# Optimization experiments

Measured on AMD Instinct MI355X. Metric: run time of the kernel, lower is better.

## Reference

```python
import jax, jax.numpy as jnp
import numpy as np

NU, NM, NT = 200000, 50000, 20000   # users, movies, tags
F, H, L = 64, 128, 2                # genre feat dim, hidden, layers
E1, E2 = 800000, 400000             # rates edges, has_tag edges


def setup_inputs() -> dict:
    key = jax.random.key(0)
    ks = jax.random.split(key, 12)
    s = 1.0 / np.sqrt(H)
    return {
        "genre": jax.random.normal(ks[0], (NM, F), jnp.float32),
        "user_emb": jax.random.normal(ks[1], (NU, H), jnp.float32),
        "tag_emb": jax.random.normal(ks[2], (NT, H), jnp.float32),
        "movie_W": jax.random.normal(ks[3], (H, F), jnp.float32) * (1.0 / np.sqrt(F)),
        "movie_b": jnp.zeros((H,), jnp.float32),
        # per-layer, per-edge-type SAGEConv weights; etype order: [rates, rev_rates, has_tag, tag_of]
        "Wn": jax.random.normal(ks[4], (L, 4, H, H), jnp.float32) * s,  # fc_neigh (no bias)
        "Ws": jax.random.normal(ks[5], (L, 4, H, H), jnp.float32) * s,  # fc_self
        "bs": jnp.zeros((L, 4, H), jnp.float32),                        # fc_self bias
        "rates_u": jax.random.randint(ks[6], (E1,), 0, NU, jnp.int32),
        "rates_m": jax.random.randint(ks[7], (E1,), 0, NM, jnp.int32),
        "tag_m": jax.random.randint(ks[8], (E2,), 0, NM, jnp.int32),
        "tag_t": jax.random.randint(ks[9], (E2,), 0, NT, jnp.int32),
    }


def _sage(h_src, h_dst, src, dst, n_dst, Wn, Wself, b):
    # DGL SAGEConv('mean'): fc_self(h_dst) + fc_neigh(mean_{src->dst} h_src)
    m = h_src[src]                                                        # [E, H] gather
    ssum = jax.ops.segment_sum(m, dst, num_segments=n_dst)                # [n_dst, H]
    cnt = jax.ops.segment_sum(jnp.ones((src.shape[0], 1), h_src.dtype), dst, num_segments=n_dst)
    mean = ssum / jnp.maximum(cnt, 1.0)                                   # zero-degree -> 0
    return h_dst @ Wself.T + b + mean @ Wn.T


def reference(genre, user_emb, tag_emb, movie_W, movie_b, Wn, Ws, bs,
              rates_u, rates_m, tag_m, tag_t):
    hu = user_emb
    hm = genre @ movie_W.T + movie_b
    ht = tag_emb
    for l in range(L):
        # HeteroGraphConv(aggregate='sum'): movie receives 'rates' + 'tag_of'
        new_m = (_sage(hu, hm, rates_u, rates_m, NM, Wn[l, 0], Ws[l, 0], bs[l, 0])
                 + _sage(ht, hm, tag_t, tag_m, NM, Wn[l, 3], Ws[l, 3], bs[l, 3]))
        new_u = _sage(hm, hu, rates_m, rates_u, NU, Wn[l, 1], Ws[l, 1], bs[l, 1])  # rev_rates
        new_t = _sage(hm, ht, tag_m, tag_t, NT, Wn[l, 2], Ws[l, 2], bs[l, 2])      # has_tag
        # dropout in eval mode (identity), then LeakyReLU(0.1)
        hu = jax.nn.leaky_relu(new_u, 0.1)
        hm = jax.nn.leaky_relu(new_m, 0.1)
        ht = jax.nn.leaky_relu(new_t, 0.1)
    return hu, hm
```

## Files before the change

### kernel.cpp

```cpp
#include <hip/hip_runtime.h>
#include <stdint.h>


#define NUSR 200000
#define NMOV 50000
#define NTAG 20000
#define FDIM 64
#define HDIM 128
#define NE1  800000
#define NE2  400000

#define OFF_RM 0
#define OFF_RU (NMOV)
#define OFF_TM (NMOV + NUSR)
#define OFF_TT (NMOV + NUSR + NMOV)
#define NTOT   (2 * NMOV + NUSR + NTAG)
#define ETOT   (2 * NE1 + 2 * NE2)
#define WHH    (HDIM * HDIM)

#define WTOT (8192 + 2 * 7 * WHH)
#define BREP 768

#define NB0 196
#define NB1 196
#define NB2 98
#define NB3 157
#define NB  (NB0 + NB1 + NB2 + NB3)
#define S1_EPB 8192
#define S1_B0 98
#define S1_B1 98
#define S1_B2 49
#define S1_B3 49
#define S1_NBLK (S1_B0 + S1_B1 + S1_B2 + S1_B3)
#define CAP 6144

typedef short bf16x8 __attribute__((ext_vector_type(8)));
typedef float f32x4 __attribute__((ext_vector_type(4)));

static inline int cdiv(int a, int b) { return (a + b - 1) / b; }

__device__ __forceinline__ float bf2f(unsigned short u) {
    union { unsigned int i; float f; } c;
    c.i = ((unsigned int)u) << 16;
    return c.f;
}
__device__ __forceinline__ unsigned short f2bf(float f) {
    union { float f; unsigned int i; } c;
    c.f = f;
    unsigned int i = c.i;
    return (unsigned short)((i + 0x7fffu + ((i >> 16) & 1u)) >> 16);
}

__device__ __forceinline__ void gload_lds16(const unsigned short* g, unsigned short* l) {
    __builtin_amdgcn_global_load_lds(
        (const __attribute__((address_space(1))) unsigned int*)(g),
        (__attribute__((address_space(3))) unsigned int*)(l), 16, 0, 0);
}

struct SegInfo {
    int e0, eN, sh, sbb, nb;
    const int* dstA;
    const int* srcA;
};
__device__ __forceinline__ SegInfo seg_decode(int blk, const int* ru, const int* rm,
                                              const int* tm, const int* tt) {
    SegInfo s;
    if (blk < S1_B0) {
        s.e0 = blk * S1_EPB; s.eN = NE1; s.sh = 8;  s.sbb = 0;                 s.nb = NB0;
        s.dstA = rm; s.srcA = ru;
    } else if (blk < S1_B0 + S1_B1) {
        s.e0 = (blk - S1_B0) * S1_EPB; s.eN = NE1; s.sh = 10; s.sbb = NB0;     s.nb = NB1;
        s.dstA = ru; s.srcA = rm;
    } else if (blk < S1_B0 + S1_B1 + S1_B2) {
        s.e0 = (blk - S1_B0 - S1_B1) * S1_EPB; s.eN = NE2; s.sh = 9;
        s.sbb = NB0 + NB1; s.nb = NB2;
        s.dstA = tm; s.srcA = tt;
    } else {
        s.e0 = (blk - S1_B0 - S1_B1 - S1_B2) * S1_EPB; s.eN = NE2; s.sh = 7;
        s.sbb = NB0 + NB1 + NB2; s.nb = NB3;
        s.dstA = tt; s.srcA = tm;
    }
    return s;
}

__global__ __launch_bounds__(256) void csr_bucket_hist(const int* __restrict__ ru,
                                                       const int* __restrict__ rm,
                                                       const int* __restrict__ tm,
                                                       const int* __restrict__ tt,
                                                       int* __restrict__ bcnt) {
    __shared__ int h[256];
    const int t = threadIdx.x;
    h[t] = 0;
    __syncthreads();
    const SegInfo s = seg_decode(blockIdx.x, ru, rm, tm, tt);
#pragma unroll 4
    for (int i = 0; i < S1_EPB / 256; ++i) {
        const int e = s.e0 + t + i * 256;
        if (e < s.eN) atomicAdd(&h[s.dstA[e] >> s.sh], 1);
    }
    __syncthreads();
    if (t < s.nb) {
        const int c = h[t];
        if (c) atomicAdd(&bcnt[s.sbb + t], c);
    }
}

__global__ __launch_bounds__(1024) void csr_bscan(const int* __restrict__ bcnt,
                                                  int* __restrict__ bbase,
                                                  int* __restrict__ bcur,
                                                  int* __restrict__ rowptr) {
    __shared__ int sh[1024];
    const int t = threadIdx.x;
    const int v = (t < NB) ? bcnt[t] : 0;
    sh[t] = v;
    __syncthreads();
    for (int off = 1; off < 1024; off <<= 1) {
        const int add = (t >= off) ? sh[t - off] : 0;
        __syncthreads();
        sh[t] += add;
        __syncthreads();
    }
    const int ex = sh[t] - v;
    if (t < NB) { bbase[t] = ex; bcur[t] = ex; }
    if (t == NB - 1) bbase[NB] = ex + v;
    if (t == 0) rowptr[NTOT] = ETOT;
}

__global__ __launch_bounds__(256) void csr_bin(const int* __restrict__ ru,
                                               const int* __restrict__ rm,
                                               const int* __restrict__ tm,
                                               const int* __restrict__ tt,
                                               int* __restrict__ bcur,
                                               int* __restrict__ tmp) {
    __shared__ int h[256], st[256], gb[256], cu[256];
    __shared__ int rec[S1_EPB];
    __shared__ unsigned short bk[S1_EPB];
    const int t = threadIdx.x;
    h[t] = 0;
    __syncthreads();
    const SegInfo s = seg_decode(blockIdx.x, ru, rm, tm, tt);
    const int mask = (1 << s.sh) - 1;
#pragma unroll 4
    for (int i = 0; i < S1_EPB / 256; ++i) {
        const int e = s.e0 + t + i * 256;
        if (e < s.eN) atomicAdd(&h[s.dstA[e] >> s.sh], 1);
    }
    __syncthreads();
    const int v = h[t];
    cu[t] = v;
    __syncthreads();
    for (int off = 1; off < 256; off <<= 1) {
        const int add = (t >= off) ? cu[t - off] : 0;
        __syncthreads();
        cu[t] += add;
        __syncthreads();
    }
    st[t] = cu[t] - v;
    gb[t] = (t < s.nb && v) ? atomicAdd(&bcur[s.sbb + t], v) : 0;
    cu[t] = st[t];
    __syncthreads();
#pragma unroll 4
    for (int i = 0; i < S1_EPB / 256; ++i) {
        const int e = s.e0 + t + i * 256;
        if (e < s.eN) {
            const int d = s.dstA[e];
            const int lb = d >> s.sh;
            const int r = ((d & mask) << 18) | s.srcA[e];
            const int p = atomicAdd(&cu[lb], 1);
            rec[p] = r;
            bk[p] = (unsigned short)lb;
        }
    }
    __syncthreads();
    const int ecount = min(S1_EPB, s.eN - s.e0);
    for (int q = t; q < ecount; q += 256) {
        const int lb = bk[q];
        tmp[gb[lb] + (q - st[lb])] = rec[q];
    }
}

__global__ __launch_bounds__(256) void csr_sort(const int* __restrict__ tmp,
                                                const int* __restrict__ bbase,
                                                int* __restrict__ rowptr,
                                                int* __restrict__ sorted) {
    __shared__ int h[1024];
    __shared__ int part[256];
    __shared__ int outb[CAP];
    const int b = blockIdx.x;
    const int t = threadIdx.x;
    int c0, nctr;
    if (b < NB0)                 { c0 = OFF_RM + (b << 8);                nctr = min(256,  NMOV - (b << 8)); }
    else if (b < NB0 + NB1)      { const int j = b - NB0;                 c0 = OFF_RU + (j << 10); nctr = min(1024, NUSR - (j << 10)); }
    else if (b < NB0 + NB1 + NB2){ const int j = b - NB0 - NB1;           c0 = OFF_TM + (j << 9);  nctr = min(512,  NMOV - (j << 9)); }
    else                         { const int j = b - NB0 - NB1 - NB2;     c0 = OFF_TT + (j << 7);  nctr = min(128,  NTAG - (j << 7)); }
    for (int k = t; k < 1024; k += 256) h[k] = 0;
    __syncthreads();
    const int lo = bbase[b], hi = bbase[b + 1];
    const int n = hi - lo;
    for (int e = lo + t; e < hi; e += 256) atomicAdd(&h[tmp[e] >> 18], 1);
    __syncthreads();
    const int b4 = t * 4;
    const int a0 = h[b4], a1 = h[b4 + 1], a2 = h[b4 + 2], a3 = h[b4 + 3];
    const int sum = a0 + a1 + a2 + a3;
    part[t] = sum;
    __syncthreads();
    for (int off = 1; off < 256; off <<= 1) {
        const int add = (t >= off) ? part[t - off] : 0;
        __syncthreads();
        part[t] += add;
        __syncthreads();
    }
    int run = part[t] - sum;
    h[b4] = run; run += a0;
    h[b4 + 1] = run; run += a1;
    h[b4 + 2] = run; run += a2;
    h[b4 + 3] = run;
    __syncthreads();
    for (int k = t; k < nctr; k += 256) rowptr[c0 + k] = lo + h[k];
    __syncthreads();
    if (n <= CAP) {
        for (int e = lo + t; e < hi; e += 256) {
            const int r = tmp[e];
            const int p = atomicAdd(&h[r >> 18], 1);
            outb[p] = r & 0x3FFFF;
        }
        __syncthreads();
        for (int q = t; q < n; q += 256) sorted[lo + q] = outb[q];
    } else {
        for (int e = lo + t; e < hi; e += 256) {
            const int r = tmp[e];
            const int p = atomicAdd(&h[r >> 18], 1);
            sorted[lo + p] = r & 0x3FFFF;
        }
    }
}

__global__ __launch_bounds__(256) void prep_all(
    const float* __restrict__ i0, unsigned short* __restrict__ o0, int n0,
    const float* __restrict__ i1, unsigned short* __restrict__ o1, int n1,
    const float* __restrict__ i2, unsigned short* __restrict__ o2, int n2,
    int gcvt,
    const float* __restrict__ movie_W, const float* __restrict__ movie_b,
    const float* __restrict__ Wn, const float* __restrict__ Ws,
    const float* __restrict__ bs,
    unsigned short* __restrict__ WB, float* __restrict__ BB) {
    if ((int)blockIdx.x < gcvt) {
        int i = blockIdx.x * 256 + threadIdx.x;
        const float* in; unsigned short* out;
        if (i < n0) { in = i0; out = o0; }
        else if (i < n0 + n1) { in = i1; out = o1; i -= n0; }
        else if (i < n0 + n1 + n2) { in = i2; out = o2; i -= n0 + n1; }
        else return;
        const float4 v = ((const float4*)in)[i];
        ushort4 o;
        o.x = f2bf(v.x); o.y = f2bf(v.y); o.z = f2bf(v.z); o.w = f2bf(v.w);
        ((ushort4*)out)[i] = o;
        return;
    }
    const int i = (blockIdx.x - gcvt) * 256 + threadIdx.x;
    if (i < BREP) {
        const int seg = i >> 7, c = i & 127;
        float bv;
        if (seg == 0)      bv = movie_b[c];
        else if (seg == 1) bv = bs[0 * 512 + 1 * 128 + c];
        else if (seg == 2) bv = bs[0 * 512 + 2 * 128 + c];
        else if (seg == 3) bv = bs[0 * 512 + 0 * 128 + c] + bs[0 * 512 + 3 * 128 + c];
        else if (seg == 4) bv = bs[1 * 512 + 1 * 128 + c];
        else               bv = bs[1 * 512 + 0 * 128 + c] + bs[1 * 512 + 3 * 128 + c];
#pragma unroll
        for (int r = 0; r < 8; ++r) BB[r * BREP + i] = bv;
    }
    if (i < WTOT) {
        float v;
        int dest;
        if (i < 8192) {
            v = movie_W[i];
            const int r0 = i >> 6, c0 = i & 63;
            dest = (r0 << 6) + ((((c0 >> 3) ^ (r0 & 7)) << 3) | (c0 & 7));
        } else {
            const int j = i - 8192;
            const int l = j / (7 * WHH);
            const int rr = j % (7 * WHH);
            const int e = rr / WHH;
            const int o = rr % WHH;
            if (e < 4) v = Wn[(l * 4 + e) * WHH + o];
            else if (e == 4) v = Ws[(l * 4 + 1) * WHH + o];
            else if (e == 5) v = Ws[(l * 4 + 2) * WHH + o];
            else v = Ws[(l * 4 + 0) * WHH + o] + Ws[(l * 4 + 3) * WHH + o];
            const int r0 = o >> 7, c0 = o & 127;
            dest = 8192 + l * 7 * WHH + e * WHH +
                   (r0 << 7) + ((((c0 >> 3) ^ (r0 & 7)) << 3) | (c0 & 7));
        }
        const unsigned short bf = f2bf(v);
#pragma unroll
        for (int r = 0; r < 8; ++r) WB[(size_t)r * WTOT + dest] = bf;
    }
}

__global__ __launch_bounds__(256) void agg4(
    const unsigned short* __restrict__ f0, const int* __restrict__ rp0, unsigned short* __restrict__ o0,
    const unsigned short* __restrict__ f1, const int* __restrict__ rp1, unsigned short* __restrict__ o1,
    const unsigned short* __restrict__ f2, const int* __restrict__ rp2, unsigned short* __restrict__ o2,
    const unsigned short* __restrict__ f3, const int* __restrict__ rp3, unsigned short* __restrict__ o3,
    int c0, int c1, int c2, int c3,
    const int* __restrict__ sorted) {
    int g = blockIdx.x * 16 + (threadIdx.x >> 4);
    const unsigned short* feat; const int* rp; unsigned short* out;
    if (g < c0) { feat = f0; rp = rp0; out = o0; }
    else if (g < c1) { feat = f1; rp = rp1; out = o1; g -= c0; }
    else if (g < c2) { feat = f2; rp = rp2; out = o2; g -= c1; }
    else if (g < c3) { feat = f3; rp = rp3; out = o3; g -= c2; }
    else return;
    const int lane = threadIdx.x & 15;
    const int s = rp[g], e = rp[g + 1];
    float a[8];
#pragma unroll
    for (int k = 0; k < 8; ++k) a[k] = 0.f;
    int j = s;
    for (; j + 1 < e; j += 2) {
        const int s0 = sorted[j], s1 = sorted[j + 1];
        const bf16x8 v0 = *(const bf16x8*)&feat[(size_t)s0 * HDIM + lane * 8];
        const bf16x8 v1 = *(const bf16x8*)&feat[(size_t)s1 * HDIM + lane * 8];
#pragma unroll
        for (int k = 0; k < 8; ++k) a[k] += bf2f((unsigned short)v0[k]) + bf2f((unsigned short)v1[k]);
    }
    if (j < e) {
        const int s0 = sorted[j];
        const bf16x8 v0 = *(const bf16x8*)&feat[(size_t)s0 * HDIM + lane * 8];
#pragma unroll
        for (int k = 0; k < 8; ++k) a[k] += bf2f((unsigned short)v0[k]);
    }
    const float sc = (e > s) ? 1.0f / (float)(e - s) : 0.0f;
    bf16x8 o;
#pragma unroll
    for (int k = 0; k < 8; ++k) o[k] = (short)f2bf(a[k] * sc);
    *(bf16x8*)&out[(size_t)g * HDIM + lane * 8] = o;
}

template <int K, bool TWO, bool HAS_ADD, bool HAS_BIAS, bool LEAKY, bool OUT_F32>
__device__ __forceinline__ void tile_core_lds(
    unsigned short* wlds,
    const unsigned short* __restrict__ X1, const unsigned short* __restrict__ W1s,
    const unsigned short* __restrict__ X2, const unsigned short* __restrict__ W2s,
    const unsigned short* __restrict__ addv, const float* __restrict__ bias,
    void* __restrict__ out, int n, int blk) {
    constexpr int NC = K / 32;
    constexpr int PASSES = (128 * K) / 2048;
    const int t = threadIdx.x;
    const int lane = t & 63;
    const int wv = t >> 6;
    const int fr = lane & 15, fq = lane >> 4;
    const int swz = fr & 7;
    const int r = blk * 64 + wv * 16 + fr;
    const int rc = (r < n) ? r : (n - 1);

#pragma unroll
    for (int p = 0; p < PASSES; ++p)
        gload_lds16(W1s + (p * 256 + t) * 8, wlds + (p * 256 + t) * 8);

    bf16x8 xf[NC];
    {
        const unsigned short* xp = X1 + (size_t)rc * K + fq * 8;
#pragma unroll
        for (int c = 0; c < NC; ++c) xf[c] = *(const bf16x8*)(xp + c * 32);
    }

    f32x4 acc[8];
#pragma unroll
    for (int nn = 0; nn < 8; ++nn) acc[nn] = (f32x4){0.f, 0.f, 0.f, 0.f};

    __syncthreads();

#pragma unroll
    for (int nn = 0; nn < 8; ++nn) {
        const int rowoff = (nn * 16 + fr) * K;
#pragma unroll
        for (int c = 0; c < NC; ++c) {
            const bf16x8 wf = *(const bf16x8*)&wlds[rowoff + (((fq + 4 * c) ^ swz) << 3)];
            acc[nn] = __builtin_amdgcn_mfma_f32_16x16x32_bf16(wf, xf[c], acc[nn], 0, 0, 0);
        }
    }

    if (TWO) {
        __syncthreads();
#pragma unroll
        for (int p = 0; p < PASSES; ++p)
            gload_lds16(W2s + (p * 256 + t) * 8, wlds + (p * 256 + t) * 8);
        {
            const unsigned short* xp = X2 + (size_t)rc * K + fq * 8;
#pragma unroll
            for (int c = 0; c < NC; ++c) xf[c] = *(const bf16x8*)(xp + c * 32);
        }
        __syncthreads();
#pragma unroll
        for (int nn = 0; nn < 8; ++nn) {
            const int rowoff = (nn * 16 + fr) * K;
#pragma unroll
            for (int c = 0; c < NC; ++c) {
                const bf16x8 wf = *(const bf16x8*)&wlds[rowoff + (((fq + 4 * c) ^ swz) << 3)];
                acc[nn] = __builtin_amdgcn_mfma_f32_16x16x32_bf16(wf, xf[c], acc[nn], 0, 0, 0);
            }
        }
    }

    if (r < n) {
#pragma unroll
        for (int nn = 0; nn < 8; ++nn) {
            const int c0 = nn * 16 + fq * 4;
            float v0 = acc[nn][0], v1 = acc[nn][1], v2 = acc[nn][2], v3 = acc[nn][3];
            if (HAS_BIAS) {
                const float4 bv = *(const float4*)&bias[c0];
                v0 += bv.x; v1 += bv.y; v2 += bv.z; v3 += bv.w;
            }
            if (HAS_ADD) {
                const ushort4 ad = *(const ushort4*)&addv[(size_t)r * HDIM + c0];
                v0 += bf2f(ad.x); v1 += bf2f(ad.y); v2 += bf2f(ad.z); v3 += bf2f(ad.w);
            }
            if (LEAKY) {
                v0 = v0 > 0.f ? v0 : 0.1f * v0;
                v1 = v1 > 0.f ? v1 : 0.1f * v1;
                v2 = v2 > 0.f ? v2 : 0.1f * v2;
                v3 = v3 > 0.f ? v3 : 0.1f * v3;
            }
            if (OUT_F32) {
                float4 o; o.x = v0; o.y = v1; o.z = v2; o.w = v3;
                *(float4*)&((float*)out)[(size_t)r * HDIM + c0] = o;
            } else {
                ushort4 o;
                o.x = f2bf(v0); o.y = f2bf(v1); o.z = f2bf(v2); o.w = f2bf(v3);
                *(ushort4*)&((unsigned short*)out)[(size_t)r * HDIM + c0] = o;
            }
        }
    }
}

__global__ __launch_bounds__(256, 5) void gemm_genre(const unsigned short* __restrict__ X,
                                                     const unsigned short* __restrict__ WB,
                                                     const float* __restrict__ BB,
                                                     unsigned short* __restrict__ out, int n) {
    __shared__ __align__(16) unsigned short wlds[128 * FDIM];
    const int rep = blockIdx.x & 7;
    tile_core_lds<FDIM, false, false, true, false, false>(
        wlds, X, WB + (size_t)rep * WTOT, nullptr, nullptr, nullptr,
        BB + rep * BREP, out, n, blockIdx.x);
}

__global__ __launch_bounds__(256, 5) void gemm_pre2(
    const unsigned short* __restrict__ Xa, unsigned short* __restrict__ oa, int na, int nba,
    const unsigned short* __restrict__ Xb, unsigned short* __restrict__ ob, int nb_,
    const unsigned short* __restrict__ WB, int offA, int offB) {
    __shared__ __align__(16) unsigned short wlds[128 * HDIM];
    const int b = blockIdx.x;
    const int rep = b & 7;
    const unsigned short* WR = WB + (size_t)rep * WTOT;
    if (b < nba)
        tile_core_lds<HDIM, false, false, false, false, false>(
            wlds, Xa, WR + offA, nullptr, nullptr, nullptr, nullptr, oa, na, b);
    else
        tile_core_lds<HDIM, false, false, false, false, false>(
            wlds, Xb, WR + offB, nullptr, nullptr, nullptr, nullptr, ob, nb_, b - nba);
}

__global__ __launch_bounds__(256, 5) void upd_l0(
    const unsigned short* __restrict__ ub, const unsigned short* __restrict__ U1v,
    unsigned short* __restrict__ U1o,
    const unsigned short* __restrict__ hm0, const unsigned short* __restrict__ M1,
    const unsigned short* __restrict__ M2v, unsigned short* __restrict__ M2o,
    const unsigned short* __restrict__ tb, const unsigned short* __restrict__ T2v,
    unsigned short* __restrict__ T3o,
    const unsigned short* __restrict__ WB, const float* __restrict__ BB,
    int gu, int gm, int gt) {
    __shared__ __align__(16) unsigned short wlds[128 * HDIM];
    const int b = blockIdx.x;
    const int rep = b & 7;
    const unsigned short* WL0 = WB + (size_t)rep * WTOT + 8192;
    const float* BR = BB + rep * BREP;
    if (b < gu) {
        tile_core_lds<HDIM, false, true, true, true, false>(
            wlds, ub, WL0 + 4 * WHH, nullptr, nullptr, U1v, BR + 128, U1o, NUSR, b);
    } else if (b < gu + gm) {
        tile_core_lds<HDIM, true, true, true, true, false>(
            wlds, hm0, WL0 + 6 * WHH, M1, WL0 + 0 * WHH, M2v, BR + 384, M2o, NMOV, b - gu);
    } else {
        tile_core_lds<HDIM, true, false, true, true, false>(
            wlds, tb, WL0 + 5 * WHH, T2v, WL0 + 2 * WHH, nullptr, BR + 256, T3o, NTAG, b - gu - gm);
    }
}

__global__ __launch_bounds__(256, 5) void upd_l1(
    const unsigned short* __restrict__ U1, const unsigned short* __restrict__ U2v,
    float* __restrict__ out_u,
    const unsigned short* __restrict__ M2, const unsigned short* __restrict__ M1,
    const unsigned short* __restrict__ M3v, float* __restrict__ out_m,
    const unsigned short* __restrict__ WB, const float* __restrict__ BB,
    int gu, int gm) {
    __shared__ __align__(16) unsigned short wlds[128 * HDIM];
    const int b = blockIdx.x;
    const int rep = b & 7;
    const unsigned short* WL1 = WB + (size_t)rep * WTOT + 8192 + 7 * WHH;
    const float* BR = BB + rep * BREP;
    if (b < gu) {
        tile_core_lds<HDIM, false, true, true, true, true>(
            wlds, U1, WL1 + 4 * WHH, nullptr, nullptr, U2v, BR + 512, out_u, NUSR, b);
    } else {
        tile_core_lds<HDIM, true, true, true, true, true>(
            wlds, M2, WL1 + 6 * WHH, M1, WL1 + 0 * WHH, M3v, BR + 640, out_m, NMOV, b - gu);
    }
}

extern "C" void kernel_launch(void* const* d_in, const int* in_sizes, int n_in,
                              void* d_out, int out_size, void* d_ws, size_t ws_size,
                              hipStream_t stream) {
    const float* genre    = (const float*)d_in[0];
    const float* user_emb = (const float*)d_in[1];
    const float* tag_emb  = (const float*)d_in[2];
    const float* movie_W  = (const float*)d_in[3];
    const float* movie_b  = (const float*)d_in[4];
    const float* Wn       = (const float*)d_in[5];
    const float* Wsf      = (const float*)d_in[6];
    const float* bsf      = (const float*)d_in[7];
    const int* rates_u    = (const int*)d_in[8];
    const int* rates_m    = (const int*)d_in[9];
    const int* tag_m      = (const int*)d_in[10];
    const int* tag_t      = (const int*)d_in[11];

    float* out_u = (float*)d_out;
    float* out_m = out_u + (size_t)NUSR * HDIM;

    char* w = (char*)d_ws;
    auto alloc = [&](size_t bytes) -> char* {
        char* p = w;
        w += (bytes + 511) & ~(size_t)511;
        return p;
    };
    unsigned short* ub  = (unsigned short*)alloc((size_t)NUSR * HDIM * 2);
    unsigned short* tb  = (unsigned short*)alloc((size_t)NTAG * HDIM * 2);
    unsigned short* gb  = (unsigned short*)alloc((size_t)NMOV * FDIM * 2);
    unsigned short* hm0 = (unsigned short*)alloc((size_t)NMOV * HDIM * 2);
    unsigned short* U1  = (unsigned short*)alloc((size_t)NUSR * HDIM * 2);
    unsigned short* M1  = (unsigned short*)alloc((size_t)NMOV * HDIM * 2);
    unsigned short* M2  = (unsigned short*)alloc((size_t)NMOV * HDIM * 2);
    unsigned short* M3  = (unsigned short*)alloc((size_t)NMOV * HDIM * 2);
    unsigned short* T1  = (unsigned short*)alloc((size_t)NTAG * HDIM * 2);
    unsigned short* T2  = (unsigned short*)alloc((size_t)NTAG * HDIM * 2);
    unsigned short* T3  = (unsigned short*)alloc((size_t)NTAG * HDIM * 2);
    unsigned short* WB  = (unsigned short*)alloc((size_t)8 * WTOT * 2);
    float* BB           = (float*)alloc((size_t)8 * BREP * 4);
    int* rowptr         = (int*)alloc((size_t)(NTOT + 1) * 4);
    int* sorted         = (int*)alloc((size_t)ETOT * 4);
    int* tmpb           = (int*)alloc((size_t)ETOT * 4);
    int* bcnt           = (int*)alloc((size_t)(NB + 1) * 4);
    int* bbase          = (int*)alloc((size_t)(NB + 1) * 4);
    int* bcur           = (int*)alloc((size_t)(NB + 1) * 4);

    const int n0 = NUSR * HDIM / 4, n1 = NTAG * HDIM / 4, n2 = NMOV * FDIM / 4;
    const int GCVT = cdiv(n0 + n1 + n2, 256);
    const int GWT  = cdiv(WTOT, 256);
    prep_all<<<GCVT + GWT, 256, 0, stream>>>(user_emb, ub, n0, tag_emb, tb, n1, genre, gb, n2,
                                             GCVT, movie_W, movie_b, Wn, Wsf, bsf, WB, BB);

    hipMemsetAsync(bcnt, 0, (size_t)(NB + 1) * 4, stream);
    csr_bucket_hist<<<S1_NBLK, 256, 0, stream>>>(rates_u, rates_m, tag_m, tag_t, bcnt);
    csr_bscan<<<1, 1024, 0, stream>>>(bcnt, bbase, bcur, rowptr);
    csr_bin<<<S1_NBLK, 256, 0, stream>>>(rates_u, rates_m, tag_m, tag_t, bcur, tmpb);
    csr_sort<<<NB, 256, 0, stream>>>(tmpb, bbase, rowptr, sorted);

    const int GU = cdiv(NUSR, 64), GM = cdiv(NMOV, 64), GT = cdiv(NTAG, 64);

    gemm_genre<<<GM, 256, 0, stream>>>(gb, WB, BB, hm0, NMOV);

    gemm_pre2<<<GM + GT, 256, 0, stream>>>(hm0, M3, NMOV, GM, tb, T1, NTAG,
                                           WB, 8192 + 1 * WHH, 8192 + 3 * WHH);
    agg4<<<cdiv(NTOT, 16), 256, 0, stream>>>(
        M3, rowptr + OFF_RU, U1,
        ub, rowptr + OFF_RM, M1,
        T1, rowptr + OFF_TM, M2,
        hm0, rowptr + OFF_TT, T2,
        NUSR, NUSR + NMOV, NUSR + 2 * NMOV, NTOT, sorted);
    upd_l0<<<GU + GM + GT, 256, 0, stream>>>(ub, U1, U1, hm0, M1, M2, M2,
                                             tb, T2, T3, WB, BB, GU, GM, GT);

    gemm_pre2<<<GM + GT, 256, 0, stream>>>(M2, M3, NMOV, GM, T3, T1, NTAG,
                                           WB, 8192 + 7 * WHH + 1 * WHH, 8192 + 7 * WHH + 3 * WHH);
    agg4<<<cdiv(NUSR + 2 * NMOV, 16), 256, 0, stream>>>(
        M3, rowptr + OFF_RU, ub,
        U1, rowptr + OFF_RM, M1,
        T1, rowptr + OFF_TM, hm0,
        nullptr, nullptr, nullptr,
        NUSR, NUSR + NMOV, NUSR + 2 * NMOV, NUSR + 2 * NMOV, sorted);
    upd_l1<<<GU + GM, 256, 0, stream>>>(U1, ub, out_u, M2, M1, hm0, out_m,
                                        WB, BB, GU, GM);
}
```

Measured before the change: 394.4 us.

## Fold CSR histogram and scan into GEMM launches; unroll gather by eight

The separate memset, bucket-histogram and single-block scan launches are merged into existing kernels. bcnt is zeroed in prep_all, the histogram blocks share a launch with the genre GEMM, and the scan runs as block 0 of the first pre-GEMM launch. This is meant to cut launch count and serialization gaps. Separately, the aggregation loop issues eight neighbor row loads at a time to raise memory-level parallelism, at the cost of more registers.

```diff
diff --git a/kernel.cpp b/kernel.cpp
--- a/kernel.cpp
+++ b/kernel.cpp
@@ -83,49 +83,6 @@
     return s;
 }
 
-__global__ __launch_bounds__(256) void csr_bucket_hist(const int* __restrict__ ru,
-                                                       const int* __restrict__ rm,
-                                                       const int* __restrict__ tm,
-                                                       const int* __restrict__ tt,
-                                                       int* __restrict__ bcnt) {
-    __shared__ int h[256];
-    const int t = threadIdx.x;
-    h[t] = 0;
-    __syncthreads();
-    const SegInfo s = seg_decode(blockIdx.x, ru, rm, tm, tt);
-#pragma unroll 4
-    for (int i = 0; i < S1_EPB / 256; ++i) {
-        const int e = s.e0 + t + i * 256;
-        if (e < s.eN) atomicAdd(&h[s.dstA[e] >> s.sh], 1);
-    }
-    __syncthreads();
-    if (t < s.nb) {
-        const int c = h[t];
-        if (c) atomicAdd(&bcnt[s.sbb + t], c);
-    }
-}
-
-__global__ __launch_bounds__(1024) void csr_bscan(const int* __restrict__ bcnt,
-                                                  int* __restrict__ bbase,
-                                                  int* __restrict__ bcur,
-                                                  int* __restrict__ rowptr) {
-    __shared__ int sh[1024];
-    const int t = threadIdx.x;
-    const int v = (t < NB) ? bcnt[t] : 0;
-    sh[t] = v;
-    __syncthreads();
-    for (int off = 1; off < 1024; off <<= 1) {
-        const int add = (t >= off) ? sh[t - off] : 0;
-        __syncthreads();
-        sh[t] += add;
-        __syncthreads();
-    }
-    const int ex = sh[t] - v;
-    if (t < NB) { bbase[t] = ex; bcur[t] = ex; }
-    if (t == NB - 1) bbase[NB] = ex + v;
-    if (t == 0) rowptr[NTOT] = ETOT;
-}
-
 __global__ __launch_bounds__(256) void csr_bin(const int* __restrict__ ru,
                                                const int* __restrict__ rm,
                                                const int* __restrict__ tm,
@@ -243,7 +200,8 @@
     const float* __restrict__ movie_W, const float* __restrict__ movie_b,
     const float* __restrict__ Wn, const float* __restrict__ Ws,
     const float* __restrict__ bs,
-    unsigned short* __restrict__ WB, float* __restrict__ BB) {
+    unsigned short* __restrict__ WB, float* __restrict__ BB,
+    int* __restrict__ bcnt) {
     if ((int)blockIdx.x < gcvt) {
         int i = blockIdx.x * 256 + threadIdx.x;
         const float* in; unsigned short* out;
@@ -258,6 +216,7 @@
         return;
     }
     const int i = (blockIdx.x - gcvt) * 256 + threadIdx.x;
+    if (i <= NB) bcnt[i] = 0;
     if (i < BREP) {
         const int seg = i >> 7, c = i & 127;
         float bv;
@@ -317,7 +276,20 @@
 #pragma unroll
     for (int k = 0; k < 8; ++k) a[k] = 0.f;
     int j = s;
-    for (; j + 1 < e; j += 2) {
+    for (; j + 8 <= e; j += 8) {
+        int si[8];
+#pragma unroll
+        for (int q = 0; q < 8; ++q) si[q] = sorted[j + q];
+        bf16x8 v[8];
+#pragma unroll
+        for (int q = 0; q < 8; ++q)
+            v[q] = *(const bf16x8*)&feat[(size_t)si[q] * HDIM + lane * 8];
+#pragma unroll
+        for (int q = 0; q < 8; ++q)
+#pragma unroll
+            for (int k = 0; k < 8; ++k) a[k] += bf2f((unsigned short)v[q][k]);
+    }
+    for (; j + 2 <= e; j += 2) {
         const int s0 = sorted[j], s1 = sorted[j + 1];
         const bf16x8 v0 = *(const bf16x8*)&feat[(size_t)s0 * HDIM + lane * 8];
         const bf16x8 v1 = *(const bf16x8*)&feat[(size_t)s1 * HDIM + lane * 8];
@@ -434,15 +406,86 @@
     }
 }
 
-__global__ __launch_bounds__(256, 5) void gemm_genre(const unsigned short* __restrict__ X,
-                                                     const unsigned short* __restrict__ WB,
-                                                     const float* __restrict__ BB,
-                                                     unsigned short* __restrict__ out, int n) {
+__global__ __launch_bounds__(256, 5) void hist_genre(
+    const int* __restrict__ ru, const int* __restrict__ rm,
+    const int* __restrict__ tm, const int* __restrict__ tt,
+    int* __restrict__ bcnt, int nhist,
+    const unsigned short* __restrict__ X, const unsigned short* __restrict__ WB,
+    const float* __restrict__ BB, unsigned short* __restrict__ out, int n) {
     __shared__ __align__(16) unsigned short wlds[128 * FDIM];
-    const int rep = blockIdx.x & 7;
+    const int b = blockIdx.x;
+    if (b < nhist) {
+        int* h = (int*)wlds;
+        const int t = threadIdx.x;
+        h[t] = 0;
+        __syncthreads();
+        const SegInfo s = seg_decode(b, ru, rm, tm, tt);
+#pragma unroll 4
+        for (int i = 0; i < S1_EPB / 256; ++i) {
+            const int e = s.e0 + t + i * 256;
+            if (e < s.eN) atomicAdd(&h[s.dstA[e] >> s.sh], 1);
+        }
+        __syncthreads();
+        if (t < s.nb) {
+            const int c = h[t];
+            if (c) atomicAdd(&bcnt[s.sbb + t], c);
+        }
+        return;
+    }
+    const int gb = b - nhist;
+    const int rep = gb & 7;
     tile_core_lds<FDIM, false, false, true, false, false>(
         wlds, X, WB + (size_t)rep * WTOT, nullptr, nullptr, nullptr,
-        BB + rep * BREP, out, n, blockIdx.x);
+        BB + rep * BREP, out, n, gb);
+}
+
+__global__ __launch_bounds__(256, 5) void bscan_pre2(
+    const int* __restrict__ bcnt, int* __restrict__ bbase, int* __restrict__ bcur,
+    int* __restrict__ rowptr,
+    const unsigned short* __restrict__ Xa, unsigned short* __restrict__ oa, int na, int nba,
+    const unsigned short* __restrict__ Xb, unsigned short* __restrict__ ob, int nb_,
+    const unsigned short* __restrict__ WB, int offA, int offB) {
+    __shared__ __align__(16) unsigned short wlds[128 * HDIM];
+    const int b = blockIdx.x;
+    if (b == 0) {
+        int* sh = (int*)wlds;
+        const int t = threadIdx.x;
+        int v[3];
+        int s = 0;
+#pragma unroll
+        for (int k = 0; k < 3; ++k) {
+            const int idx = t * 3 + k;
+            v[k] = (idx < NB) ? bcnt[idx] : 0;
+            s += v[k];
+        }
+        sh[t] = s;
+        __syncthreads();
+        for (int off = 1; off < 256; off <<= 1) {
+            const int add = (t >= off) ? sh[t - off] : 0;
+            __syncthreads();
+            sh[t] += add;
+            __syncthreads();
+        }
+        int run = sh[t] - s;
+#pragma unroll
+        for (int k = 0; k < 3; ++k) {
+            const int idx = t * 3 + k;
+            if (idx < NB) { bbase[idx] = run; bcur[idx] = run; }
+            run += v[k];
+        }
+        if (t == 255) bbase[NB] = run;
+        if (t == 0) rowptr[NTOT] = ETOT;
+        return;
+    }
+    const int pb = b - 1;
+    const int rep = pb & 7;
+    const unsigned short* WR = WB + (size_t)rep * WTOT;
+    if (pb < nba)
+        tile_core_lds<HDIM, false, false, false, false, false>(
+            wlds, Xa, WR + offA, nullptr, nullptr, nullptr, nullptr, oa, na, pb);
+    else
+        tile_core_lds<HDIM, false, false, false, false, false>(
+            wlds, Xb, WR + offB, nullptr, nullptr, nullptr, nullptr, ob, nb_, pb - nba);
 }
 
 __global__ __launch_bounds__(256, 5) void gemm_pre2(
@@ -553,24 +596,24 @@
     int* bbase          = (int*)alloc((size_t)(NB + 1) * 4);
     int* bcur           = (int*)alloc((size_t)(NB + 1) * 4);
 
+    const int GU = cdiv(NUSR, 64), GM = cdiv(NMOV, 64), GT = cdiv(NTAG, 64);
+
     const int n0 = NUSR * HDIM / 4, n1 = NTAG * HDIM / 4, n2 = NMOV * FDIM / 4;
     const int GCVT = cdiv(n0 + n1 + n2, 256);
     const int GWT  = cdiv(WTOT, 256);
     prep_all<<<GCVT + GWT, 256, 0, stream>>>(user_emb, ub, n0, tag_emb, tb, n1, genre, gb, n2,
-                                             GCVT, movie_W, movie_b, Wn, Wsf, bsf, WB, BB);
-
-    hipMemsetAsync(bcnt, 0, (size_t)(NB + 1) * 4, stream);
-    csr_bucket_hist<<<S1_NBLK, 256, 0, stream>>>(rates_u, rates_m, tag_m, tag_t, bcnt);
-    csr_bscan<<<1, 1024, 0, stream>>>(bcnt, bbase, bcur, rowptr);
+                                             GCVT, movie_W, movie_b, Wn, Wsf, bsf, WB, BB, bcnt);
+
+    hist_genre<<<S1_NBLK + GM, 256, 0, stream>>>(rates_u, rates_m, tag_m, tag_t, bcnt, S1_NBLK,
+                                                 gb, WB, BB, hm0, NMOV);
+
+    bscan_pre2<<<1 + GM + GT, 256, 0, stream>>>(bcnt, bbase, bcur, rowptr,
+                                                hm0, M3, NMOV, GM, tb, T1, NTAG,
+                                                WB, 8192 + 1 * WHH, 8192 + 3 * WHH);
+
     csr_bin<<<S1_NBLK, 256, 0, stream>>>(rates_u, rates_m, tag_m, tag_t, bcur, tmpb);
     csr_sort<<<NB, 256, 0, stream>>>(tmpb, bbase, rowptr, sorted);
 
-    const int GU = cdiv(NUSR, 64), GM = cdiv(NMOV, 64), GT = cdiv(NTAG, 64);
-
-    gemm_genre<<<GM, 256, 0, stream>>>(gb, WB, BB, hm0, NMOV);
-
-    gemm_pre2<<<GM + GT, 256, 0, stream>>>(hm0, M3, NMOV, GM, tb, T1, NTAG,
-                                           WB, 8192 + 1 * WHH, 8192 + 3 * WHH);
     agg4<<<cdiv(NTOT, 16), 256, 0, stream>>>(
         M3, rowptr + OFF_RU, U1,
         ub, rowptr + OFF_RM, M1,
```

Result: slower. 407.3 us (+3.3%).
